# Performance work log

Hardware: AMD Instinct MI355X
Metric: run time of the kernel (lower is better)

Reference implementation:

```python
import jax, jax.numpy as jnp
import numpy as np

BT, L, F, N = 8, 8192, 128, 16


def setup_inputs() -> dict:
    key = jax.random.key(0)
    ks = jax.random.split(key, 7)
    scale = 1.0 / np.sqrt(F)
    x = jax.random.normal(ks[0], (BT, L, F), dtype=jnp.float32)
    Wb = jax.random.normal(ks[1], (F, N), dtype=jnp.float32) * scale
    bb = jax.random.normal(ks[2], (N,), dtype=jnp.float32) * 0.01
    Wc = jax.random.normal(ks[3], (F, N), dtype=jnp.float32) * scale
    bc = jax.random.normal(ks[4], (N,), dtype=jnp.float32) * 0.01
    Wd = jax.random.normal(ks[5], (F, 1), dtype=jnp.float32) * scale
    bd = jax.random.normal(ks[6], (1,), dtype=jnp.float32) * 0.01
    # diagonal HiPPO-like spectrum (A is diagonal in the source: torch.diag(eigenvalues))
    A = -(jnp.arange(N, dtype=jnp.float32) + 1.0)
    return {"x": x, "Wb": Wb, "bb": bb, "Wc": Wc, "bc": bc, "Wd": Wd, "bd": bd, "A": A}


def reference(x, Wb, bb, Wc, bc, Wd, bd, A):
    # input-dependent SSM parameters (S6 / selective scan)
    B = x @ Wb + bb                      # [BT, L, N]
    C = x @ Wc + bc                      # [BT, L, N]
    delta = jax.nn.softplus(x @ Wd + bd)  # [BT, L, 1]
    # ZOH discretization with diagonal A
    dA = jnp.exp(delta * A)              # [BT, L, N]
    dB = (dA - 1.0) / A * B              # [BT, L, N]

    def step(h, inp):
        dA_t, dB_t, x_t, C_t = inp       # [BT,N],[BT,N],[BT,F],[BT,N]
        # h: [BT, F, N]; each feature channel has its own N-dim state
        h = dA_t[:, None, :] * h + dB_t[:, None, :] * x_t[:, :, None]
        y = jnp.einsum('bfn,bn->bf', h, C_t)
        return h, y

    h0 = jnp.zeros((x.shape[0], x.shape[2], A.shape[0]), dtype=x.dtype)
    xs = (jnp.swapaxes(dA, 0, 1), jnp.swapaxes(dB, 0, 1),
          jnp.swapaxes(x, 0, 1), jnp.swapaxes(C, 0, 1))
    _, ys = jax.lax.scan(step, h0, xs)   # ys: [L, BT, F]
    return jnp.swapaxes(ys, 0, 1)        # [BT, L, F]
```

## Files before the change

### kernel.cpp

```cpp
#include <hip/hip_runtime.h>


#define BTc   8
#define Lseq  8192
#define Fdim  128
#define Ndim  16
#define CH    128
#define LC    64

__global__ __launch_bounds__(256) void k_pre(
    const float* __restrict__ x,
    const float* __restrict__ Wb, const float* __restrict__ bb,
    const float* __restrict__ Wc, const float* __restrict__ bc,
    const float* __restrict__ Wd, const float* __restrict__ bd,
    const float* __restrict__ A,  float* __restrict__ G,
    float* __restrict__ S)
{
    __shared__ float Wl[33][4][36];
    __shared__ float Dl[2][64];
    const int tid = threadIdx.x;
    for (int idx = tid; idx < 33 * 128; idx += 256) {
        int j = idx >> 7, k = idx & 127;
        float v;
        if (j < 16)      v = Wb[k * 16 + j];
        else if (j < 32) v = Wc[k * 16 + (j - 16)];
        else             v = Wd[k];
        Wl[j][k >> 5][k & 31] = v;
    }
    __syncthreads();

    const int t2 = tid >> 2, ks = tid & 3;
    const size_t tokA = (size_t)blockIdx.x * 128 + t2;
    const float4* xA = reinterpret_cast<const float4*>(x + tokA * 128 + ks * 32);
    const float4* xB = reinterpret_cast<const float4*>(x + (tokA + 64) * 128 + ks * 32);

    float accA[33], accB[33];
#pragma unroll
    for (int j = 0; j < 33; ++j) { accA[j] = 0.f; accB[j] = 0.f; }

#pragma unroll 2
    for (int kk = 0; kk < 8; ++kk) {
        float4 a = xA[kk], b = xB[kk];
#pragma unroll
        for (int j = 0; j < 33; ++j) {
            float4 w = *reinterpret_cast<const float4*>(&Wl[j][ks][kk * 4]);
            accA[j] = fmaf(a.x, w.x, accA[j]);
            accA[j] = fmaf(a.y, w.y, accA[j]);
            accA[j] = fmaf(a.z, w.z, accA[j]);
            accA[j] = fmaf(a.w, w.w, accA[j]);
            accB[j] = fmaf(b.x, w.x, accB[j]);
            accB[j] = fmaf(b.y, w.y, accB[j]);
            accB[j] = fmaf(b.z, w.z, accB[j]);
            accB[j] = fmaf(b.w, w.w, accB[j]);
        }
    }

    float sel[33];
#pragma unroll
    for (int j = 0; j < 33; ++j) {
        accA[j] += __shfl_xor(accA[j], 1);
        accA[j] += __shfl_xor(accA[j], 2);
        accB[j] += __shfl_xor(accB[j], 1);
        accB[j] += __shfl_xor(accB[j], 2);
        sel[j] = (ks & 1) ? accB[j] : accA[j];
    }

    if (ks < 2) {
        const size_t tok = tokA + (size_t)(ks & 1) * 64;
        float v = sel[32] + bd[0];
        float delta = fmaxf(v, 0.f) + log1pf(expf(-fabsf(v)));
        Dl[ks][t2] = delta;
        float out[48];
#pragma unroll
        for (int n = 0; n < 16; ++n) {
            float An = A[n];
            float dA = expf(delta * An);
            float dB = (dA - 1.f) / An * (sel[n] + bb[n]);
            out[n]      = dA;
            out[16 + n] = dB;
            out[32 + n] = sel[16 + n] + bc[n];
        }
        float4* Gr = reinterpret_cast<float4*>(G + tok * 48);
#pragma unroll
        for (int p = 0; p < 12; ++p)
            Gr[p] = make_float4(out[4*p], out[4*p+1], out[4*p+2], out[4*p+3]);
    }
    __syncthreads();

    if (tid < 128) {
        float val = Dl[tid >> 6][tid & 63];
#pragma unroll
        for (int m = 1; m < 64; m <<= 1) val += __shfl_xor(val, m);
        if ((tid & 63) == 0) S[blockIdx.x * 2 + (tid >> 6)] = val;
    }
}

__global__ __launch_bounds__(128, 2) void k_local(
    const float* __restrict__ x, const float* __restrict__ G,
    float* __restrict__ q)
{
    __shared__ float Gl[LC][32];
    const int c = blockIdx.x, b = blockIdx.y;
    const int f = threadIdx.x;
    const size_t tok0 = (size_t)b * Lseq + (size_t)c * LC;

    const float4* Gg = reinterpret_cast<const float4*>(G + tok0 * 48);
    float4* Gs = reinterpret_cast<float4*>(&Gl[0][0]);
    for (int idx = f; idx < LC * 8; idx += 128) {
        int t = idx >> 3, p = idx & 7;
        Gs[idx] = Gg[t * 12 + p];
    }
    __syncthreads();

    float h[16];
#pragma unroll
    for (int n = 0; n < 16; ++n) h[n] = 0.f;

    const float* xp = x + tok0 * Fdim + f;
#pragma unroll 2
    for (int t = 0; t < LC; ++t) {
        float xv = xp[t * Fdim];
        const float4* gp4 = reinterpret_cast<const float4*>(&Gl[t][0]);
        float da[16], db[16];
#pragma unroll
        for (int p = 0; p < 4; ++p) {
            float4 va = gp4[p], vb = gp4[4 + p];
            da[4*p] = va.x; da[4*p+1] = va.y; da[4*p+2] = va.z; da[4*p+3] = va.w;
            db[4*p] = vb.x; db[4*p+1] = vb.y; db[4*p+2] = vb.z; db[4*p+3] = vb.w;
        }
#pragma unroll
        for (int n = 0; n < 16; ++n)
            h[n] = fmaf(da[n], h[n], db[n] * xv);
    }

    float4* qp = reinterpret_cast<float4*>(q + ((size_t)(b * CH + c) * 128 + f) * 16);
#pragma unroll
    for (int n4 = 0; n4 < 4; ++n4)
        qp[n4] = make_float4(h[4*n4], h[4*n4+1], h[4*n4+2], h[4*n4+3]);
}

__global__ __launch_bounds__(256) void k_chunkscan(
    const float* __restrict__ q, const float* __restrict__ S,
    const float* __restrict__ A, float* __restrict__ Hin)
{
    int id = blockIdx.x * 256 + threadIdx.x;
    int b  = id >> 11;
    int fn = id & 2047;
    int n  = id & 15;
    float An = A[n];
    float H = 0.f;
    size_t qb = (size_t)b * CH * 2048 + fn;
    const float* Sb = S + b * CH;
    for (int cg = 0; cg < CH; cg += 16) {
        float Sr[16], qr[16];
#pragma unroll
        for (int i = 0; i < 16; ++i) {
            Sr[i] = Sb[cg + i];
            qr[i] = q[qb + (size_t)(cg + i) * 2048];
        }
#pragma unroll
        for (int i = 0; i < 16; ++i) {
            Hin[qb + (size_t)(cg + i) * 2048] = H;
            H = fmaf(__expf(An * Sr[i]), H, qr[i]);
        }
    }
}

__global__ __launch_bounds__(128, 2) void k_final(
    const float* __restrict__ x, const float* __restrict__ G,
    const float* __restrict__ Hin, float* __restrict__ y)
{
    __shared__ float Gl[LC][48];
    const int c = blockIdx.x, b = blockIdx.y;
    const int f = threadIdx.x;
    const size_t tok0 = (size_t)b * Lseq + (size_t)c * LC;

    const float4* Gg = reinterpret_cast<const float4*>(G + tok0 * 48);
    float4* Gs = reinterpret_cast<float4*>(&Gl[0][0]);
    for (int idx = f; idx < LC * 12; idx += 128)
        Gs[idx] = Gg[idx];
    __syncthreads();

    float h[16];
    const float4* hp = reinterpret_cast<const float4*>(Hin + ((size_t)(b * CH + c) * 128 + f) * 16);
#pragma unroll
    for (int n4 = 0; n4 < 4; ++n4) {
        float4 v = hp[n4];
        h[4*n4] = v.x; h[4*n4+1] = v.y; h[4*n4+2] = v.z; h[4*n4+3] = v.w;
    }

    const float* xp = x + tok0 * Fdim + f;
    float*       yp = y + tok0 * Fdim + f;
#pragma unroll 2
    for (int t = 0; t < LC; ++t) {
        float xv = xp[t * Fdim];
        const float4* gp4 = reinterpret_cast<const float4*>(&Gl[t][0]);
        float da[16], db[16], cc[16];
#pragma unroll
        for (int p = 0; p < 4; ++p) {
            float4 va = gp4[p], vb = gp4[4 + p], vc = gp4[8 + p];
            da[4*p] = va.x; da[4*p+1] = va.y; da[4*p+2] = va.z; da[4*p+3] = va.w;
            db[4*p] = vb.x; db[4*p+1] = vb.y; db[4*p+2] = vb.z; db[4*p+3] = vb.w;
            cc[4*p] = vc.x; cc[4*p+1] = vc.y; cc[4*p+2] = vc.z; cc[4*p+3] = vc.w;
        }
        float yacc = 0.f;
#pragma unroll
        for (int n = 0; n < 16; ++n) {
            h[n] = fmaf(da[n], h[n], db[n] * xv);
            yacc = fmaf(cc[n], h[n], yacc);
        }
        yp[t * Fdim] = yacc;
    }
}

extern "C" void kernel_launch(void* const* d_in, const int* in_sizes, int n_in,
                              void* d_out, int out_size, void* d_ws, size_t ws_size,
                              hipStream_t stream) {
    const float* x  = (const float*)d_in[0];
    const float* Wb = (const float*)d_in[1];
    const float* bb = (const float*)d_in[2];
    const float* Wc = (const float*)d_in[3];
    const float* bc = (const float*)d_in[4];
    const float* Wd = (const float*)d_in[5];
    const float* bd = (const float*)d_in[6];
    const float* A  = (const float*)d_in[7];
    float* y = (float*)d_out;

    float* G   = (float*)d_ws;
    float* q   = G   + (size_t)BTc * Lseq * 48;
    float* Hin = q   + (size_t)BTc * CH * Fdim * Ndim;
    float* S   = Hin + (size_t)BTc * CH * Fdim * Ndim;

    k_pre<<<dim3(512), 256, 0, stream>>>(x, Wb, bb, Wc, bc, Wd, bd, A, G, S);
    k_local<<<dim3(CH, BTc), 128, 0, stream>>>(x, G, q);
    k_chunkscan<<<dim3(BTc * Fdim * Ndim / 256), 256, 0, stream>>>(q, S, A, Hin);
    k_final<<<dim3(CH, BTc), 128, 0, stream>>>(x, G, Hin, y);
}
```

Measured before the change: 80.43 us.

## Compute local outputs in first scan pass and add cheap carry-in correction

Measured after the change: 94.33 us. 1.17x slower.

```diff
diff --git a/kernel.cpp b/kernel.cpp
--- a/kernel.cpp
+++ b/kernel.cpp
@@ -14,10 +14,11 @@
     const float* __restrict__ Wc, const float* __restrict__ bc,
     const float* __restrict__ Wd, const float* __restrict__ bd,
     const float* __restrict__ A,  float* __restrict__ G,
-    float* __restrict__ S)
+    float* __restrict__ E, float* __restrict__ S)
 {
     __shared__ float Wl[33][4][36];
     __shared__ float Dl[2][64];
+    __shared__ float Cum[2][64];
     const int tid = threadIdx.x;
     for (int idx = tid; idx < 33 * 128; idx += 256) {
         int j = idx >> 7, k = idx & 127;
@@ -30,7 +31,8 @@
     __syncthreads();
 
     const int t2 = tid >> 2, ks = tid & 3;
-    const size_t tokA = (size_t)blockIdx.x * 128 + t2;
+    const size_t gtok0 = (size_t)blockIdx.x * 128;
+    const size_t tokA = gtok0 + t2;
     const float4* xA = reinterpret_cast<const float4*>(x + tokA * 128 + ks * 32);
     const float4* xB = reinterpret_cast<const float4*>(x + (tokA + 64) * 128 + ks * 32);
 
@@ -65,8 +67,9 @@
         sel[j] = (ks & 1) ? accB[j] : accA[j];
     }
 
+    float Cv[16];
     if (ks < 2) {
-        const size_t tok = tokA + (size_t)(ks & 1) * 64;
+        const size_t tok = gtok0 + (size_t)ks * 64 + t2;
         float v = sel[32] + bd[0];
         float delta = fmaxf(v, 0.f) + log1pf(expf(-fabsf(v)));
         Dl[ks][t2] = delta;
@@ -75,10 +78,10 @@
         for (int n = 0; n < 16; ++n) {
             float An = A[n];
             float dA = expf(delta * An);
-            float dB = (dA - 1.f) / An * (sel[n] + bb[n]);
+            Cv[n] = sel[16 + n] + bc[n];
             out[n]      = dA;
-            out[16 + n] = dB;
-            out[32 + n] = sel[16 + n] + bc[n];
+            out[16 + n] = (dA - 1.f) / An * (sel[n] + bb[n]);
+            out[32 + n] = Cv[n];
         }
         float4* Gr = reinterpret_cast<float4*>(G + tok * 48);
 #pragma unroll
@@ -88,55 +91,84 @@
     __syncthreads();
 
     if (tid < 128) {
-        float val = Dl[tid >> 6][tid & 63];
-#pragma unroll
-        for (int m = 1; m < 64; m <<= 1) val += __shfl_xor(val, m);
-        if ((tid & 63) == 0) S[blockIdx.x * 2 + (tid >> 6)] = val;
-    }
-}
-
-__global__ __launch_bounds__(128, 2) void k_local(
+        const int w = tid >> 6, lane = tid & 63;
+        float cum = Dl[w][lane];
+#pragma unroll
+        for (int off = 1; off < 64; off <<= 1) {
+            float up = __shfl_up(cum, off);
+            cum += (lane >= off) ? up : 0.f;
+        }
+        Cum[w][lane] = cum;
+        if (lane == 63) S[blockIdx.x * 2 + w] = cum;
+    }
+    __syncthreads();
+
+    if (ks < 2) {
+        const size_t chunk = (size_t)blockIdx.x * 2 + ks;
+        float cumv = Cum[ks][t2];
+        float Ev[16];
+#pragma unroll
+        for (int n = 0; n < 16; ++n)
+            Ev[n] = Cv[n] * expf(A[n] * cumv);
+        float4* Ep = reinterpret_cast<float4*>(E + (chunk * 64 + t2) * 16);
+#pragma unroll
+        for (int p = 0; p < 4; ++p)
+            Ep[p] = make_float4(Ev[4*p], Ev[4*p+1], Ev[4*p+2], Ev[4*p+3]);
+    }
+}
+
+__global__ __launch_bounds__(64) void k_scan(
     const float* __restrict__ x, const float* __restrict__ G,
-    float* __restrict__ q)
-{
-    __shared__ float Gl[LC][32];
+    float* __restrict__ y, float* __restrict__ q)
+{
+    __shared__ float Gl[LC][48];
     const int c = blockIdx.x, b = blockIdx.y;
-    const int f = threadIdx.x;
+    const int lane = threadIdx.x;
     const size_t tok0 = (size_t)b * Lseq + (size_t)c * LC;
 
     const float4* Gg = reinterpret_cast<const float4*>(G + tok0 * 48);
     float4* Gs = reinterpret_cast<float4*>(&Gl[0][0]);
-    for (int idx = f; idx < LC * 8; idx += 128) {
-        int t = idx >> 3, p = idx & 7;
-        Gs[idx] = Gg[t * 12 + p];
-    }
-    __syncthreads();
-
-    float h[16];
-#pragma unroll
-    for (int n = 0; n < 16; ++n) h[n] = 0.f;
-
-    const float* xp = x + tok0 * Fdim + f;
+    for (int idx = lane; idx < LC * 12; idx += 64) Gs[idx] = Gg[idx];
+    __syncthreads();
+
+    float h0[16], h1[16];
+#pragma unroll
+    for (int n = 0; n < 16; ++n) { h0[n] = 0.f; h1[n] = 0.f; }
+
+    const float* xs = x + tok0 * Fdim;
+    float*       yp = y + tok0 * Fdim;
 #pragma unroll 2
     for (int t = 0; t < LC; ++t) {
-        float xv = xp[t * Fdim];
+        float xv0 = xs[t * Fdim + lane];
+        float xv1 = xs[t * Fdim + lane + 64];
         const float4* gp4 = reinterpret_cast<const float4*>(&Gl[t][0]);
-        float da[16], db[16];
+        float da[16], db[16], cc[16];
 #pragma unroll
         for (int p = 0; p < 4; ++p) {
-            float4 va = gp4[p], vb = gp4[4 + p];
+            float4 va = gp4[p], vb = gp4[4 + p], vc = gp4[8 + p];
             da[4*p] = va.x; da[4*p+1] = va.y; da[4*p+2] = va.z; da[4*p+3] = va.w;
             db[4*p] = vb.x; db[4*p+1] = vb.y; db[4*p+2] = vb.z; db[4*p+3] = vb.w;
-        }
-#pragma unroll
-        for (int n = 0; n < 16; ++n)
-            h[n] = fmaf(da[n], h[n], db[n] * xv);
-    }
-
-    float4* qp = reinterpret_cast<float4*>(q + ((size_t)(b * CH + c) * 128 + f) * 16);
-#pragma unroll
-    for (int n4 = 0; n4 < 4; ++n4)
-        qp[n4] = make_float4(h[4*n4], h[4*n4+1], h[4*n4+2], h[4*n4+3]);
+            cc[4*p] = vc.x; cc[4*p+1] = vc.y; cc[4*p+2] = vc.z; cc[4*p+3] = vc.w;
+        }
+        float y0 = 0.f, y1 = 0.f;
+#pragma unroll
+        for (int n = 0; n < 16; ++n) {
+            h0[n] = fmaf(da[n], h0[n], db[n] * xv0);
+            h1[n] = fmaf(da[n], h1[n], db[n] * xv1);
+            y0 = fmaf(cc[n], h0[n], y0);
+            y1 = fmaf(cc[n], h1[n], y1);
+        }
+        yp[t * Fdim + lane]      = y0;
+        yp[t * Fdim + lane + 64] = y1;
+    }
+
+    float4* qp0 = reinterpret_cast<float4*>(q + ((size_t)(b * CH + c) * Fdim + lane) * 16);
+    float4* qp1 = reinterpret_cast<float4*>(q + ((size_t)(b * CH + c) * Fdim + lane + 64) * 16);
+#pragma unroll
+    for (int p = 0; p < 4; ++p) {
+        qp0[p] = make_float4(h0[4*p], h0[4*p+1], h0[4*p+2], h0[4*p+3]);
+        qp1[p] = make_float4(h1[4*p], h1[4*p+1], h1[4*p+2], h1[4*p+3]);
+    }
 }
 
 __global__ __launch_bounds__(256) void k_chunkscan(
@@ -166,50 +198,44 @@
     }
 }
 
-__global__ __launch_bounds__(128, 2) void k_final(
-    const float* __restrict__ x, const float* __restrict__ G,
-    const float* __restrict__ Hin, float* __restrict__ y)
-{
-    __shared__ float Gl[LC][48];
+__global__ __launch_bounds__(64) void k_correct(
+    const float* __restrict__ Hin, const float* __restrict__ E,
+    float* __restrict__ y)
+{
+    __shared__ float El[LC][16];
     const int c = blockIdx.x, b = blockIdx.y;
-    const int f = threadIdx.x;
-    const size_t tok0 = (size_t)b * Lseq + (size_t)c * LC;
-
-    const float4* Gg = reinterpret_cast<const float4*>(G + tok0 * 48);
-    float4* Gs = reinterpret_cast<float4*>(&Gl[0][0]);
-    for (int idx = f; idx < LC * 12; idx += 128)
-        Gs[idx] = Gg[idx];
-    __syncthreads();
-
-    float h[16];
-    const float4* hp = reinterpret_cast<const float4*>(Hin + ((size_t)(b * CH + c) * 128 + f) * 16);
-#pragma unroll
-    for (int n4 = 0; n4 < 4; ++n4) {
-        float4 v = hp[n4];
-        h[4*n4] = v.x; h[4*n4+1] = v.y; h[4*n4+2] = v.z; h[4*n4+3] = v.w;
-    }
-
-    const float* xp = x + tok0 * Fdim + f;
-    float*       yp = y + tok0 * Fdim + f;
+    const int lane = threadIdx.x;
+
+    const float4* Eg = reinterpret_cast<const float4*>(E + (size_t)(b * CH + c) * LC * 16);
+    float4* Es = reinterpret_cast<float4*>(&El[0][0]);
+    for (int i = lane; i < LC * 4; i += 64) Es[i] = Eg[i];
+
+    float hv0[16], hv1[16];
+    const float4* hp0 = reinterpret_cast<const float4*>(Hin + ((size_t)(b * CH + c) * Fdim + lane) * 16);
+    const float4* hp1 = reinterpret_cast<const float4*>(Hin + ((size_t)(b * CH + c) * Fdim + lane + 64) * 16);
+#pragma unroll
+    for (int p = 0; p < 4; ++p) {
+        float4 a = hp0[p], bb4 = hp1[p];
+        hv0[4*p] = a.x; hv0[4*p+1] = a.y; hv0[4*p+2] = a.z; hv0[4*p+3] = a.w;
+        hv1[4*p] = bb4.x; hv1[4*p+1] = bb4.y; hv1[4*p+2] = bb4.z; hv1[4*p+3] = bb4.w;
+    }
+    __syncthreads();
+
+    float* yp = y + ((size_t)b * Lseq + (size_t)c * LC) * Fdim;
 #pragma unroll 2
     for (int t = 0; t < LC; ++t) {
-        float xv = xp[t * Fdim];
-        const float4* gp4 = reinterpret_cast<const float4*>(&Gl[t][0]);
-        float da[16], db[16], cc[16];
+        const float4* ep = reinterpret_cast<const float4*>(&El[t][0]);
+        float a0 = 0.f, a1 = 0.f;
 #pragma unroll
         for (int p = 0; p < 4; ++p) {
-            float4 va = gp4[p], vb = gp4[4 + p], vc = gp4[8 + p];
-            da[4*p] = va.x; da[4*p+1] = va.y; da[4*p+2] = va.z; da[4*p+3] = va.w;
-            db[4*p] = vb.x; db[4*p+1] = vb.y; db[4*p+2] = vb.z; db[4*p+3] = vb.w;
-            cc[4*p] = vc.x; cc[4*p+1] = vc.y; cc[4*p+2] = vc.z; cc[4*p+3] = vc.w;
-        }
-        float yacc = 0.f;
-#pragma unroll
-        for (int n = 0; n < 16; ++n) {
-            h[n] = fmaf(da[n], h[n], db[n] * xv);
-            yacc = fmaf(cc[n], h[n], yacc);
-        }
-        yp[t * Fdim] = yacc;
+            float4 e4 = ep[p];
+            a0 = fmaf(e4.x, hv0[4*p],   a0); a1 = fmaf(e4.x, hv1[4*p],   a1);
+            a0 = fmaf(e4.y, hv0[4*p+1], a0); a1 = fmaf(e4.y, hv1[4*p+1], a1);
+            a0 = fmaf(e4.z, hv0[4*p+2], a0); a1 = fmaf(e4.z, hv1[4*p+2], a1);
+            a0 = fmaf(e4.w, hv0[4*p+3], a0); a1 = fmaf(e4.w, hv1[4*p+3], a1);
+        }
+        yp[t * Fdim + lane]      += a0;
+        yp[t * Fdim + lane + 64] += a1;
     }
 }
 
@@ -229,10 +255,11 @@
     float* G   = (float*)d_ws;
     float* q   = G   + (size_t)BTc * Lseq * 48;
     float* Hin = q   + (size_t)BTc * CH * Fdim * Ndim;
-    float* S   = Hin + (size_t)BTc * CH * Fdim * Ndim;
-
-    k_pre<<<dim3(512), 256, 0, stream>>>(x, Wb, bb, Wc, bc, Wd, bd, A, G, S);
-    k_local<<<dim3(CH, BTc), 128, 0, stream>>>(x, G, q);
+    float* E   = Hin + (size_t)BTc * CH * Fdim * Ndim;
+    float* S   = E   + (size_t)BTc * Lseq * Ndim;
+
+    k_pre<<<dim3(512), 256, 0, stream>>>(x, Wb, bb, Wc, bc, Wd, bd, A, G, E, S);
+    k_scan<<<dim3(CH, BTc), 64, 0, stream>>>(x, G, y, q);
     k_chunkscan<<<dim3(BTc * Fdim * Ndim / 256), 256, 0, stream>>>(q, S, A, Hin);
-    k_final<<<dim3(CH, BTc), 128, 0, stream>>>(x, G, Hin, y);
-}
+    k_correct<<<dim3(CH, BTc), 64, 0, stream>>>(Hin, E, y);
+}
```
